# Kernel optimization log

Hardware: AMD Instinct MI355X
Metric: run time of the kernel (lower is better)

## Reference

```python
import jax, jax.numpy as jnp
import numpy as np

NUM_PTS = 1024
LATENT_SIZE = 32
BETA = 0.1


def setup_inputs() -> dict:
    key = jax.random.key(0)
    k1, k2, k3, k4 = jax.random.split(key, 4)
    B = 128
    return {
        "recon_x": jax.random.normal(k1, (B, NUM_PTS, 3), dtype=jnp.float32),
        "x": jax.random.normal(k2, (B, NUM_PTS, 3), dtype=jnp.float32),
        "mu": jax.random.normal(k3, (B, LATENT_SIZE), dtype=jnp.float32),
        "logvar": jax.random.normal(k4, (B, LATENT_SIZE), dtype=jnp.float32),
    }


def _chamfer(recon_x, x):
    # Batched squared pairwise distances: P[b, i, j] = ||x[b,i] - recon_x[b,j]||^2
    xx = jnp.sum(x * x, axis=-1)              # [B, N]
    yy = jnp.sum(recon_x * recon_x, axis=-1)  # [B, N]
    xy = jnp.einsum("bnd,bmd->bnm", x, recon_x)  # [B, N, N]
    P = xx[:, :, None] + yy[:, None, :] - 2.0 * xy
    # Bidirectional min + sum
    loss_1 = jnp.sum(jnp.min(P, axis=1))  # for each recon point, nearest x point
    loss_2 = jnp.sum(jnp.min(P, axis=2))  # for each x point, nearest recon point
    return loss_1 + loss_2


def reference(recon_x, x, mu, logvar):
    RE = _chamfer(recon_x, x) / NUM_PTS
    KLD = -0.5 * jnp.sum(1.0 + logvar - mu * mu - jnp.exp(logvar))
    KLD = KLD / LATENT_SIZE
    return RE + KLD * BETA
```

## Files before the change

kernel.cpp:

```cpp
#include <hip/hip_runtime.h>

#define NUM_PTS 1024
#define NBATCH 128
#define BT 256
#define RT 256
#define NJC 8
#define JCH 64
#define R 16
#define CHAMF_SCALE (1.0f / 1024.0f)
#define KLD_SCALE   (-0.5f * 0.1f / 32.0f)

#define WS_CHUNK (NBATCH * NUM_PTS)
#define WS_DIR   (NJC * WS_CHUNK)

__global__ __launch_bounds__(BT, 2) void chamfer_part(
    const float* __restrict__ recon_x,
    const float* __restrict__ x,
    float* __restrict__ ws,
    float* __restrict__ out)
{
    const int b  = blockIdx.x & 127;
    const int c  = blockIdx.x >> 7;
    const int w  = threadIdx.x >> 6;
    const int lt = threadIdx.x & 63;
    const int dir  = w & 1;
    const int half = w >> 1;

    if (blockIdx.x == 0 && threadIdx.x == 0) out[0] = 0.0f;

    __shared__ float sq[4][4][JCH];
    __shared__ float comb[2][NUM_PTS + 64];

    {
        const float* qsrc = (dir == 0 ? recon_x : x)
            + (size_t)b * NUM_PTS * 3 + (size_t)(c * 128 + half * JCH + lt) * 3;
        const float qx = qsrc[0], qy = qsrc[1], qz = qsrc[2];
        sq[w][0][lt] = qx;
        sq[w][1][lt] = qy;
        sq[w][2][lt] = qz;
        sq[w][3][lt] = fmaf(qx, qx, fmaf(qy, qy, qz * qz));
    }

    const float* rp = (dir == 0 ? x : recon_x) + (size_t)b * NUM_PTS * 3;
    float vx[R], vy[R], vz[R], m[R];
    {
        float buf[48];
        const float4* __restrict__ s4 = (const float4*)(rp + 48 * lt);
        float4* bp = (float4*)buf;
#pragma unroll
        for (int i = 0; i < 12; ++i) bp[i] = s4[i];
#pragma unroll
        for (int k = 0; k < R; ++k) {
            vx[k] = -2.0f * buf[3 * k + 0];
            vy[k] = -2.0f * buf[3 * k + 1];
            vz[k] = -2.0f * buf[3 * k + 2];
            m[k]  = 1e30f;
        }
    }

    const float4* __restrict__ qxp = (const float4*)sq[w][0];
    const float4* __restrict__ qyp = (const float4*)sq[w][1];
    const float4* __restrict__ qzp = (const float4*)sq[w][2];
    const float4* __restrict__ q2p = (const float4*)sq[w][3];
#pragma unroll 2
    for (int g = 0; g < JCH / 4; ++g) {
        const float4 qx = qxp[g];
        const float4 qy = qyp[g];
        const float4 qz = qzp[g];
        const float4 q2 = q2p[g];
#pragma unroll
        for (int r = 0; r < R; ++r) {
            const float d0 = fmaf(vx[r], qx.x, fmaf(vy[r], qy.x, fmaf(vz[r], qz.x, q2.x)));
            const float d1 = fmaf(vx[r], qx.y, fmaf(vy[r], qy.y, fmaf(vz[r], qz.y, q2.y)));
            m[r] = fminf(fminf(m[r], d0), d1);
        }
#pragma unroll
        for (int r = 0; r < R; ++r) {
            const float d2 = fmaf(vx[r], qx.z, fmaf(vy[r], qy.z, fmaf(vz[r], qz.z, q2.z)));
            const float d3 = fmaf(vx[r], qx.w, fmaf(vy[r], qy.w, fmaf(vz[r], qz.w, q2.w)));
            m[r] = fminf(fminf(m[r], d2), d3);
        }
    }

    if (half == 0) {
#pragma unroll
        for (int k = 0; k < R; ++k)
            comb[dir][17 * lt + k] = m[k];
    }
    __syncthreads();
    if (half == 1) {
        float4* dst = (float4*)(ws + (size_t)dir * WS_DIR + (size_t)c * WS_CHUNK
                                + b * NUM_PTS + 16 * lt);
#pragma unroll
        for (int k4 = 0; k4 < 4; ++k4) {
            float o[4];
#pragma unroll
            for (int i = 0; i < 4; ++i) {
                const int k = 4 * k4 + i;
                const float mm = fminf(m[k], comb[dir][17 * lt + k]);
                const float r2 = 0.25f * fmaf(vx[k], vx[k],
                                        fmaf(vy[k], vy[k], vz[k] * vz[k]));
                o[i] = r2 + mm;
            }
            dst[k4] = make_float4(o[0], o[1], o[2], o[3]);
        }
    }
}

__global__ __launch_bounds__(RT) void reduce_kernel(
    const float* __restrict__ ws,
    const float* __restrict__ mu,
    const float* __restrict__ logvar,
    float* __restrict__ out)
{
    const int gid  = blockIdx.x * RT + threadIdx.x;
    const int base = gid * 4;
    const int dir  = base >> 17;
    const int rem  = base & 131071;

    const float4* p = (const float4*)(ws + (size_t)dir * WS_DIR + rem);
    float4 mn = p[0];
#pragma unroll
    for (int c = 1; c < NJC; ++c) {
        const float4 q = p[c * (WS_CHUNK / 4)];
        mn.x = fminf(mn.x, q.x);
        mn.y = fminf(mn.y, q.y);
        mn.z = fminf(mn.z, q.z);
        mn.w = fminf(mn.w, q.w);
    }
    float v = (mn.x + mn.y + mn.z + mn.w) * CHAMF_SCALE;

    if (blockIdx.x < 16) {
        const int t = blockIdx.x * RT + threadIdx.x;
        const float lv = logvar[t];
        const float mm = mu[t];
        v += (1.0f + lv - mm * mm - expf(lv)) * KLD_SCALE;
    }

    for (int off = 32; off > 0; off >>= 1)
        v += __shfl_down(v, off, 64);

    __shared__ float red[RT / 64];
    const int lane = threadIdx.x & 63;
    const int wv   = threadIdx.x >> 6;
    if (lane == 0) red[wv] = v;
    __syncthreads();
    if (threadIdx.x == 0) {
        float sum = 0.f;
        for (int wq = 0; wq < RT / 64; ++wq) sum += red[wq];
        atomicAdd(out, sum);
    }
}

extern "C" void kernel_launch(void* const* d_in, const int* in_sizes, int n_in,
                              void* d_out, int out_size, void* d_ws, size_t ws_size,
                              hipStream_t stream) {
    const float* recon_x = (const float*)d_in[0];
    const float* x       = (const float*)d_in[1];
    const float* mu      = (const float*)d_in[2];
    const float* logvar  = (const float*)d_in[3];
    float* out = (float*)d_out;
    float* ws  = (float*)d_ws;

    chamfer_part<<<NBATCH * NJC, BT, 0, stream>>>(recon_x, x, ws, out);
    reduce_kernel<<<256, RT, 0, stream>>>(ws, mu, logvar, out);
}
```

Before: 88.19 us.

## Fuse chamfer min-combine and sum into main kernel, shrink final reduction

Restructures the work split so each block handles one direction, one batch and half of the reference points, while its 8 waves each scan a 128-point query slice. Per-point minima are then combined across waves in shared memory and summed inside the block. This removes the large per-chunk workspace write and the 256-block reduction pass that re-read it, leaving a single-block final reduction that also computes the KLD term and drops the atomic. Registers per thread are halved (R=8) to allow more waves, at the cost of less reuse of each query load per thread.

```diff
diff --git a/kernel.cpp b/kernel.cpp
--- a/kernel.cpp
+++ b/kernel.cpp
@@ -2,53 +2,54 @@
 
 #define NUM_PTS 1024
 #define NBATCH 128
-#define BT 256
-#define RT 256
-#define NJC 8
-#define JCH 64
-#define R 16
+#define BT 512
+#define NW 8
+#define QW 128
+#define R 8
 #define CHAMF_SCALE (1.0f / 1024.0f)
 #define KLD_SCALE   (-0.5f * 0.1f / 32.0f)
 
-#define WS_CHUNK (NBATCH * NUM_PTS)
-#define WS_DIR   (NJC * WS_CHUNK)
-
-__global__ __launch_bounds__(BT, 2) void chamfer_part(
+__global__ __launch_bounds__(BT, 4) void chamfer_fused(
     const float* __restrict__ recon_x,
     const float* __restrict__ x,
-    float* __restrict__ ws,
-    float* __restrict__ out)
+    float* __restrict__ ws)
 {
-    const int b  = blockIdx.x & 127;
-    const int c  = blockIdx.x >> 7;
-    const int w  = threadIdx.x >> 6;
-    const int lt = threadIdx.x & 63;
-    const int dir  = w & 1;
-    const int half = w >> 1;
+    const int bid = blockIdx.x;
+    const int dir = bid & 1;
+    const int b   = (bid >> 1) & 127;
+    const int rh  = bid >> 8;
+    const int w   = threadIdx.x >> 6;
+    const int lt  = threadIdx.x & 63;
 
-    if (blockIdx.x == 0 && threadIdx.x == 0) out[0] = 0.0f;
-
-    __shared__ float sq[4][4][JCH];
-    __shared__ float comb[2][NUM_PTS + 64];
+    __shared__ float sq[NW][4][QW];
+    __shared__ float comb[NW][BT];
+    __shared__ float red[NW];
 
     {
         const float* qsrc = (dir == 0 ? recon_x : x)
-            + (size_t)b * NUM_PTS * 3 + (size_t)(c * 128 + half * JCH + lt) * 3;
-        const float qx = qsrc[0], qy = qsrc[1], qz = qsrc[2];
-        sq[w][0][lt] = qx;
-        sq[w][1][lt] = qy;
-        sq[w][2][lt] = qz;
-        sq[w][3][lt] = fmaf(qx, qx, fmaf(qy, qy, qz * qz));
+            + (size_t)b * NUM_PTS * 3 + (size_t)(w * QW) * 3;
+#pragma unroll
+        for (int i = 0; i < 2; ++i) {
+            const int p = i * 64 + lt;
+            const float qx = qsrc[3 * p + 0];
+            const float qy = qsrc[3 * p + 1];
+            const float qz = qsrc[3 * p + 2];
+            sq[w][0][p] = qx;
+            sq[w][1][p] = qy;
+            sq[w][2][p] = qz;
+            sq[w][3][p] = fmaf(qx, qx, fmaf(qy, qy, qz * qz));
+        }
     }
 
-    const float* rp = (dir == 0 ? x : recon_x) + (size_t)b * NUM_PTS * 3;
+    const float* rp = (dir == 0 ? x : recon_x)
+        + (size_t)b * NUM_PTS * 3 + (size_t)rh * 512 * 3;
     float vx[R], vy[R], vz[R], m[R];
     {
-        float buf[48];
-        const float4* __restrict__ s4 = (const float4*)(rp + 48 * lt);
+        float buf[24];
+        const float4* __restrict__ s4 = (const float4*)(rp + 24 * lt);
         float4* bp = (float4*)buf;
 #pragma unroll
-        for (int i = 0; i < 12; ++i) bp[i] = s4[i];
+        for (int i = 0; i < 6; ++i) bp[i] = s4[i];
 #pragma unroll
         for (int k = 0; k < R; ++k) {
             vx[k] = -2.0f * buf[3 * k + 0];
@@ -63,7 +64,7 @@
     const float4* __restrict__ qzp = (const float4*)sq[w][2];
     const float4* __restrict__ q2p = (const float4*)sq[w][3];
 #pragma unroll 2
-    for (int g = 0; g < JCH / 4; ++g) {
+    for (int g = 0; g < QW / 4; ++g) {
         const float4 qx = qxp[g];
         const float4 qy = qyp[g];
         const float4 qz = qzp[g];
@@ -82,73 +83,64 @@
         }
     }
 
-    if (half == 0) {
 #pragma unroll
-        for (int k = 0; k < R; ++k)
-            comb[dir][17 * lt + k] = m[k];
+    for (int k = 0; k < R; ++k) {
+        const float r2 = 0.25f * fmaf(vx[k], vx[k], fmaf(vy[k], vy[k], vz[k] * vz[k]));
+        comb[w][8 * lt + k] = m[k] + r2;
     }
     __syncthreads();
-    if (half == 1) {
-        float4* dst = (float4*)(ws + (size_t)dir * WS_DIR + (size_t)c * WS_CHUNK
-                                + b * NUM_PTS + 16 * lt);
+
+    const int t = threadIdx.x;
+    float v = comb[0][t];
 #pragma unroll
-        for (int k4 = 0; k4 < 4; ++k4) {
-            float o[4];
+    for (int ww = 1; ww < NW; ++ww) v = fminf(v, comb[ww][t]);
+
+    for (int off = 32; off > 0; off >>= 1)
+        v += __shfl_down(v, off, 64);
+    if (lt == 0) red[w] = v;
+    __syncthreads();
+    if (t == 0) {
+        float s = 0.0f;
 #pragma unroll
-            for (int i = 0; i < 4; ++i) {
-                const int k = 4 * k4 + i;
-                const float mm = fminf(m[k], comb[dir][17 * lt + k]);
-                const float r2 = 0.25f * fmaf(vx[k], vx[k],
-                                        fmaf(vy[k], vy[k], vz[k] * vz[k]));
-                o[i] = r2 + mm;
-            }
-            dst[k4] = make_float4(o[0], o[1], o[2], o[3]);
-        }
+        for (int ww = 0; ww < NW; ++ww) s += red[ww];
+        ws[bid] = s;
     }
 }
 
-__global__ __launch_bounds__(RT) void reduce_kernel(
+__global__ __launch_bounds__(BT) void final_reduce(
     const float* __restrict__ ws,
     const float* __restrict__ mu,
     const float* __restrict__ logvar,
     float* __restrict__ out)
 {
-    const int gid  = blockIdx.x * RT + threadIdx.x;
-    const int base = gid * 4;
-    const int dir  = base >> 17;
-    const int rem  = base & 131071;
+    const int t = threadIdx.x;
+    float v = ws[t] * CHAMF_SCALE;
 
-    const float4* p = (const float4*)(ws + (size_t)dir * WS_DIR + rem);
-    float4 mn = p[0];
+    const float4* mp = (const float4*)mu + 2 * t;
+    const float4* lp = (const float4*)logvar + 2 * t;
+    float kv = 0.0f;
 #pragma unroll
-    for (int c = 1; c < NJC; ++c) {
-        const float4 q = p[c * (WS_CHUNK / 4)];
-        mn.x = fminf(mn.x, q.x);
-        mn.y = fminf(mn.y, q.y);
-        mn.z = fminf(mn.z, q.z);
-        mn.w = fminf(mn.w, q.w);
+    for (int i = 0; i < 2; ++i) {
+        const float4 mm = mp[i];
+        const float4 lv = lp[i];
+        kv += (1.0f + lv.x - mm.x * mm.x - expf(lv.x));
+        kv += (1.0f + lv.y - mm.y * mm.y - expf(lv.y));
+        kv += (1.0f + lv.z - mm.z * mm.z - expf(lv.z));
+        kv += (1.0f + lv.w - mm.w * mm.w - expf(lv.w));
     }
-    float v = (mn.x + mn.y + mn.z + mn.w) * CHAMF_SCALE;
-
-    if (blockIdx.x < 16) {
-        const int t = blockIdx.x * RT + threadIdx.x;
-        const float lv = logvar[t];
-        const float mm = mu[t];
-        v += (1.0f + lv - mm * mm - expf(lv)) * KLD_SCALE;
-    }
+    v += kv * KLD_SCALE;
 
     for (int off = 32; off > 0; off >>= 1)
         v += __shfl_down(v, off, 64);
 
-    __shared__ float red[RT / 64];
-    const int lane = threadIdx.x & 63;
-    const int wv   = threadIdx.x >> 6;
-    if (lane == 0) red[wv] = v;
+    __shared__ float red[BT / 64];
+    if ((t & 63) == 0) red[t >> 6] = v;
     __syncthreads();
-    if (threadIdx.x == 0) {
-        float sum = 0.f;
-        for (int wq = 0; wq < RT / 64; ++wq) sum += red[wq];
-        atomicAdd(out, sum);
+    if (t == 0) {
+        float s = 0.0f;
+#pragma unroll
+        for (int ww = 0; ww < BT / 64; ++ww) s += red[ww];
+        out[0] = s;
     }
 }
 
@@ -162,6 +154,6 @@
     float* out = (float*)d_out;
     float* ws  = (float*)d_ws;
 
-    chamfer_part<<<NBATCH * NJC, BT, 0, stream>>>(recon_x, x, ws, out);
-    reduce_kernel<<<256, RT, 0, stream>>>(ws, mu, logvar, out);
+    chamfer_fused<<<512, BT, 0, stream>>>(recon_x, x, ws);
+    final_reduce<<<1, BT, 0, stream>>>(ws, mu, logvar, out);
 }
```

Result: faster. 80.12 us (-9.2%).
